# Kernel optimization log

Measured on AMD Instinct MI355X. Metric: run time of the kernel, lower is better.

## Reference

```python
import jax, jax.numpy as jnp
import numpy as np

NB = 4          # bits per symbol (QAM16)
K = 3           # num_streams
M = 8           # rx antennas
B = 4096        # batch
NPTS = 2 ** NB  # constellation points per stream
C = NPTS ** K   # exhaustive candidate vectors


def _pam_gray(b):
    if len(b) > 1:
        return (1 - 2 * b[0]) * (2 ** len(b[1:]) - _pam_gray(b[1:]))
    return 1 - 2 * b[0]


def _qam_points(nb):
    # Gray-labeled QAM, normalized to unit average energy (as sionna's Constellation)
    n = 2 ** nb
    pts = np.zeros(n, np.complex64)
    for i in range(n):
        b = np.array(list(np.binary_repr(i, nb)), int)
        pts[i] = _pam_gray(b[0::2]) + 1j * _pam_gray(b[1::2])
    pts /= np.sqrt(np.mean(np.abs(pts) ** 2)).astype(np.float32)
    return pts.astype(np.complex64)


def _candidates():
    pts = _qam_points(NB)
    idx = np.arange(C)
    # per-stream symbol indices, stream 0 is most significant (vec_list order)
    sym_idx = np.stack([(idx // NPTS ** (K - 1 - k)) % NPTS for k in range(K)], axis=1)  # [C,K]
    xc = pts[sym_idx]  # [C,K] complex candidate symbol vectors
    # bits: MSB-first per symbol -> [C, K, NB]
    bits = ((sym_idx[..., None] >> (NB - 1 - np.arange(NB))) & 1).astype(bool)
    return xc, bits.reshape(C, K * NB)


_XC, _BITS = _candidates()


def setup_inputs() -> dict:
    key = jax.random.key(0)
    ks = jax.random.split(key, 6)
    y_re = jax.random.normal(ks[0], (B, M), jnp.float32)
    y_im = jax.random.normal(ks[1], (B, M), jnp.float32)
    h_re = jax.random.normal(ks[2], (B, M, K), jnp.float32)
    h_im = jax.random.normal(ks[3], (B, M, K), jnp.float32)
    # Hermitian PD noise covariance S = F F^H / M + 2 I
    fr = jax.random.normal(ks[4], (B, M, M), jnp.float32)
    fi = jax.random.normal(ks[5], (B, M, M), jnp.float32)
    F = fr + 1j * fi
    S = jnp.einsum('bij,bkj->bik', F, F.conj()) / M + 2.0 * jnp.eye(M, dtype=jnp.complex64)
    return {"y_re": y_re, "y_im": y_im, "h_re": h_re, "h_im": h_im,
            "s_re": jnp.real(S), "s_im": jnp.imag(S)}


def reference(y_re, y_im, h_re, h_im, s_re, s_im):
    y = y_re + 1j * y_im            # [B,M]
    h = h_re + 1j * h_im            # [B,M,K]
    s = s_re + 1j * s_im            # [B,M,M] Hermitian PD
    # Whiten: L L^H = S ; ||L^{-1}(y - Hx)||^2 = (y-Hx)^H S^{-1} (y-Hx)
    L = jnp.linalg.cholesky(s)
    yw = jax.scipy.linalg.solve_triangular(L, y[..., None], lower=True)[..., 0]  # [B,M]
    hw = jax.scipy.linalg.solve_triangular(L, h, lower=True)                     # [B,M,K]

    xc = jnp.asarray(_XC)                         # [C,K]
    G = jnp.einsum('bmk,bml->bkl', hw.conj(), hw)  # [B,K,K] Gram
    z = jnp.einsum('bm,bmk->bk', yw.conj(), hw)    # [B,K]  y~^H H~
    P = xc.conj()[:, :, None] * xc[:, None, :]     # [C,K,K] candidate outer products
    quad = jnp.real(jnp.einsum('bkl,ckl->bc', G, P))   # x^H G x
    cross = jnp.real(jnp.einsum('bk,ck->bc', z, xc))   # Re(y~^H H~ x)
    yn = jnp.sum(jnp.abs(yw) ** 2, axis=-1, keepdims=True)
    d = yn - 2.0 * cross + quad                   # [B,C] exhaustive squared distances

    # maxlog bit LLRs: LLR = min_{bit=0} d - min_{bit=1} d
    bits = jnp.asarray(_BITS)                     # [C, K*NB] bool
    BIG = jnp.float32(1e30)
    llrs = []
    for p in range(K * NB):  # fixed small loop over bit positions
        mask = bits[:, p]
        min1 = jnp.min(jnp.where(mask, d, BIG), axis=1)
        min0 = jnp.min(jnp.where(mask, BIG, d), axis=1)
        llrs.append(min0 - min1)
    return jnp.stack(llrs, axis=-1).reshape(B, K, NB)
```

## Files before the change

kernel.cpp:

```cpp
#include <hip/hip_runtime.h>
#include <math.h>

#define BIG 1e30f
#define RT10 0.31622776601683794f

__device__ __forceinline__ constexpr float QR(int i) {
    return ((((i >> 3) & 1) ? -1.0f : 1.0f) * ((((i >> 1) & 1) ? 3.0f : 1.0f)) * RT10);
}
__device__ __forceinline__ constexpr float QI(int i) {
    return ((((i >> 2) & 1) ? -1.0f : 1.0f) * (((i & 1) ? 3.0f : 1.0f)) * RT10);
}

__global__ __launch_bounds__(256) void mld_wave(
    const float* __restrict__ y_re, const float* __restrict__ y_im,
    const float* __restrict__ h_re, const float* __restrict__ h_im,
    const float* __restrict__ s_re, const float* __restrict__ s_im,
    float* __restrict__ out, int B) {
    int tid = threadIdx.x;
    int w = tid >> 6, lane = tid & 63;
    int b = blockIdx.x * 4 + w;
    bool live = (b < B);
    if (!live) b = B - 1;

    __shared__ float s_xr[4][4][8], s_xi[4][4][8];
    __shared__ float s_w[4][16];
    __shared__ float s16[4][16];

    {
        int ii = lane >> 3, kk = lane & 7;
        float ar = s_re[b * 64 + lane];
        float ai = s_im[b * 64 + lane];
        float br = 0.0f, bi = 0.0f;
        if (kk == 0) {
            br = y_re[b * 8 + ii];
            bi = y_im[b * 8 + ii];
        } else if (kk < 4) {
            br = h_re[b * 24 + ii * 3 + (kk - 1)];
            bi = h_im[b * 24 + ii * 3 + (kk - 1)];
        }

#pragma unroll
        for (int j = 0; j < 8; ++j) {
            float djr = __shfl(ar, j * 9, 64);
            float dinv = 1.0f / sqrtf(djr);
            if (kk == j && ii >= j) { ar *= dinv; ai *= dinv; }
            float Lijr = __shfl(ar, ii * 8 + j, 64), Liji = __shfl(ai, ii * 8 + j, 64);
            float Lkjr = __shfl(ar, kk * 8 + j, 64), Lkji = __shfl(ai, kk * 8 + j, 64);
            if (kk > j && ii >= kk) {
                ar -= Lijr * Lkjr + Liji * Lkji;
                ai -= Liji * Lkjr - Lijr * Lkji;
            }
        }
#pragma unroll
        for (int k = 0; k < 8; ++k) {
            float dk = __shfl(ar, k * 9, 64);
            float dinvk = 1.0f / dk;
            if (ii == k) { br *= dinvk; bi *= dinvk; }
            float xkr = __shfl(br, k * 8 + kk, 64), xki = __shfl(bi, k * 8 + kk, 64);
            float Likr = __shfl(ar, ii * 8 + k, 64), Liki = __shfl(ai, ii * 8 + k, 64);
            if (ii > k) {
                br -= Likr * xkr - Liki * xki;
                bi -= Likr * xki + Liki * xkr;
            }
        }
        if (kk < 4) { s_xr[w][kk][ii] = br; s_xi[w][kk][ii] = bi; }
    }
    __syncthreads();

    if (lane < 9) {
        int pa = (int)((0x000211321ull >> (lane * 4)) & 15ull);
        int pc = (int)((0x321332321ull >> (lane * 4)) & 15ull);
        float sr = 0.0f, si = 0.0f;
#pragma unroll
        for (int m = 0; m < 8; ++m) {
            float xar = s_xr[w][pa][m], xai = s_xi[w][pa][m];
            float xbr = s_xr[w][pc][m], xbi = s_xi[w][pc][m];
            sr += xar * xbr + xai * xbi;
            si += xar * xbi - xai * xbr;
        }
        if (lane < 3) {
            s_w[w][lane] = sr;
        } else {
            int base2 = 3 + (lane - 3) * 2;
            s_w[w][base2] = sr;
            s_w[w][base2 + 1] = si;
        }
    }
    __syncthreads();

    const float* ww = s_w[w];
    float g00 = ww[0], g11 = ww[1], g22 = ww[2];
    float g01r = ww[3], g01i = ww[4], g02r = ww[5], g02i = ww[6];
    float g12r = ww[7], g12i = ww[8];
    float z0r = ww[9], z0i = ww[10], z1r = ww[11], z1i = ww[12];
    float z2r = ww[13], z2i = ww[14];

    int a = lane >> 4, i1 = lane & 15;
    float p1r = QR(i1), p1i = QI(i1);
    float n1 = p1r * p1r + p1i * p1i;
    float a1c = g11 * n1 - 2.0f * (z1r * p1r - z1i * p1i);
    float w1r = g12r * p1r + g12i * p1i;
    float w1i = g12i * p1r - g12r * p1i;
    float mr0 = (a & 2) ? 3.0f * RT10 : RT10;
    float mi0 = (a & 1) ? 3.0f * RT10 : RT10;
    float n0 = mr0 * mr0 + mi0 * mi0;
    float g00n0 = g00 * n0;

    float ch[12];
#pragma unroll
    for (int j = 0; j < 12; ++j) ch[j] = BIG;
    float u[4];
#pragma unroll
    for (int q = 0; q < 4; ++q) {
        float p0r = (q & 2) ? -mr0 : mr0;
        float p0i = (q & 1) ? -mi0 : mi0;
        float a0c = g00n0 - 2.0f * (z0r * p0r - z0i * p0i);
        float crr = p0r * p1r + p0i * p1i;
        float cri = p0r * p1i - p0i * p1r;
        float base = a0c + a1c + 2.0f * (g01r * crr - g01i * cri);
        float w0r = g02r * p0r + g02i * p0i;
        float w0i = g02i * p0r - g02r * p0i;
        float cr = 2.0f * (w0r + w1r - z2r);
        float ci = -2.0f * (w0i + w1i - z2i);
        float bA = fmaf(g22, 0.2f, base);
        float bB = fmaf(g22, 1.0f, base);
        float bC = fmaf(g22, 1.8f, base);
        float pmin = BIG;
#pragma unroll
        for (int i2 = 0; i2 < 16; ++i2) {
            int cls = ((i2 >> 1) & 1) + (i2 & 1);
            float bX = (cls == 0) ? bA : (cls == 1 ? bB : bC);
            float d = fmaf(QI(i2), ci, fmaf(QR(i2), cr, bX));
            pmin = fminf(pmin, d);
            ch[0 + ((i2 >> 3) & 1)] = fminf(ch[0 + ((i2 >> 3) & 1)], d);
            ch[2 + ((i2 >> 2) & 1)] = fminf(ch[2 + ((i2 >> 2) & 1)], d);
            ch[4 + ((i2 >> 1) & 1)] = fminf(ch[4 + ((i2 >> 1) & 1)], d);
            ch[6 + (i2 & 1)]        = fminf(ch[6 + (i2 & 1)], d);
        }
        u[q] = pmin;
    }
    ch[8] = fminf(u[0], u[1]);
    ch[9] = fminf(u[2], u[3]);
    ch[10] = fminf(u[0], u[2]);
    ch[11] = fminf(u[1], u[3]);

#pragma unroll
    for (int j = 0; j < 12; ++j) {
        float v = ch[j];
#pragma unroll
        for (int mask = 1; mask < 64; mask <<= 1) v = fminf(v, __shfl_xor(v, mask, 64));
        ch[j] = v;
    }

    float t1 = fminf(fminf(u[0], u[1]), fminf(u[2], u[3]));
    float r0 = t1;
#pragma unroll
    for (int mask = 1; mask <= 8; mask <<= 1) r0 = fminf(r0, __shfl_xor(r0, mask, 64));
    float r1 = fminf(t1, __shfl_xor(t1, 16, 64));
    r1 = fminf(r1, __shfl_xor(r1, 32, 64));
    if (lane < 16) s16[w][lane] = r1;

    float zv = fminf(r0, __shfl_xor(r0, 16, 64));
    float llr2 = zv - __shfl_xor(zv, 32, 64);
    float yv = fminf(r0, __shfl_xor(r0, 32, 64));
    float llr3 = yv - __shfl_xor(yv, 16, 64);
    __syncthreads();

    if (live) {
        float* ob = out + b * 12;
        if (lane == 0) {
            ob[0] = ch[8] - ch[9];
            ob[1] = ch[10] - ch[11];
            ob[2] = llr2;
            ob[3] = llr3;
        } else if (lane >= 4 && lane < 8) {
            int k = 3 - (lane - 4);
            float m0 = BIG, m1 = BIG;
#pragma unroll
            for (int j = 0; j < 16; ++j) {
                float v = s16[w][j];
                if ((j >> k) & 1) m1 = fminf(m1, v);
                else m0 = fminf(m0, v);
            }
            ob[lane] = m0 - m1;
        } else if (lane >= 8 && lane < 12) {
            int n = lane - 8;
            ob[lane] = ch[n * 2] - ch[n * 2 + 1];
        }
    }
}

extern "C" void kernel_launch(void* const* d_in, const int* in_sizes, int n_in,
                              void* d_out, int out_size, void* d_ws, size_t ws_size,
                              hipStream_t stream) {
    const float* y_re = (const float*)d_in[0];
    const float* y_im = (const float*)d_in[1];
    const float* h_re = (const float*)d_in[2];
    const float* h_im = (const float*)d_in[3];
    const float* s_re = (const float*)d_in[4];
    const float* s_im = (const float*)d_in[5];
    int B = in_sizes[0] / 8;

    mld_wave<<<dim3((B + 3) / 4), dim3(256), 0, stream>>>(y_re, y_im, h_re, h_im,
                                                          s_re, s_im, (float*)d_out, B);
}
```

Measured before the change: 76.66 us.

## Separate innermost QAM search into independent real/imag minima and use fast rcp/rsq

Replaces the 16-point inner enumeration over the third stream's symbol with a closed form. The distance splits into a real-part term and an imaginary-part term, each minimized over the two PAM amplitudes and signs, so the bit-conditioned minima come from a few fmins and abs operations instead of 16 distance evaluations per candidate. Per-candidate constants are hoisted out of the q loop. It also swaps the IEEE divide and sqrt in the Cholesky and triangular solve for hardware rsq/rcp intrinsics, which may slightly change LLR precision.

```diff
diff --git a/kernel.cpp b/kernel.cpp
--- a/kernel.cpp
+++ b/kernel.cpp
@@ -42,7 +42,7 @@
 #pragma unroll
         for (int j = 0; j < 8; ++j) {
             float djr = __shfl(ar, j * 9, 64);
-            float dinv = 1.0f / sqrtf(djr);
+            float dinv = __builtin_amdgcn_rsqf(djr);
             if (kk == j && ii >= j) { ar *= dinv; ai *= dinv; }
             float Lijr = __shfl(ar, ii * 8 + j, 64), Liji = __shfl(ai, ii * 8 + j, 64);
             float Lkjr = __shfl(ar, kk * 8 + j, 64), Lkji = __shfl(ai, kk * 8 + j, 64);
@@ -54,7 +54,7 @@
 #pragma unroll
         for (int k = 0; k < 8; ++k) {
             float dk = __shfl(ar, k * 9, 64);
-            float dinvk = 1.0f / dk;
+            float dinvk = __builtin_amdgcn_rcpf(dk);
             if (ii == k) { br *= dinvk; bi *= dinvk; }
             float xkr = __shfl(br, k * 8 + kk, 64), xki = __shfl(bi, k * 8 + kk, 64);
             float Likr = __shfl(ar, ii * 8 + k, 64), Liki = __shfl(ai, ii * 8 + k, 64);
@@ -104,7 +104,15 @@
     float mr0 = (a & 2) ? 3.0f * RT10 : RT10;
     float mi0 = (a & 1) ? 3.0f * RT10 : RT10;
     float n0 = mr0 * mr0 + mi0 * mi0;
-    float g00n0 = g00 * n0;
+
+    float C0 = fmaf(g00, n0, a1c);
+    float P = 2.0f * mr0 * (g01r * p1r - g01i * p1i - z0r);
+    float Q = 2.0f * mi0 * (g01r * p1i + g01i * p1r + z0i);
+    float cw = 2.0f * (w1r - z2r);
+    float cv = 2.0f * (z2i - w1i);
+    float gr1 = 2.0f * g02r * mr0, gr2 = 2.0f * g02i * mi0;
+    float gi1 = 2.0f * g02i * mr0, gi2 = 2.0f * g02r * mi0;
+    float gA = 0.1f * g22, gB = 0.9f * g22;
 
     float ch[12];
 #pragma unroll
@@ -112,32 +120,31 @@
     float u[4];
 #pragma unroll
     for (int q = 0; q < 4; ++q) {
-        float p0r = (q & 2) ? -mr0 : mr0;
-        float p0i = (q & 1) ? -mi0 : mi0;
-        float a0c = g00n0 - 2.0f * (z0r * p0r - z0i * p0i);
-        float crr = p0r * p1r + p0i * p1i;
-        float cri = p0r * p1i - p0i * p1r;
-        float base = a0c + a1c + 2.0f * (g01r * crr - g01i * cri);
-        float w0r = g02r * p0r + g02i * p0i;
-        float w0i = g02i * p0r - g02r * p0i;
-        float cr = 2.0f * (w0r + w1r - z2r);
-        float ci = -2.0f * (w0i + w1i - z2i);
-        float bA = fmaf(g22, 0.2f, base);
-        float bB = fmaf(g22, 1.0f, base);
-        float bC = fmaf(g22, 1.8f, base);
-        float pmin = BIG;
-#pragma unroll
-        for (int i2 = 0; i2 < 16; ++i2) {
-            int cls = ((i2 >> 1) & 1) + (i2 & 1);
-            float bX = (cls == 0) ? bA : (cls == 1 ? bB : bC);
-            float d = fmaf(QI(i2), ci, fmaf(QR(i2), cr, bX));
-            pmin = fminf(pmin, d);
-            ch[0 + ((i2 >> 3) & 1)] = fminf(ch[0 + ((i2 >> 3) & 1)], d);
-            ch[2 + ((i2 >> 2) & 1)] = fminf(ch[2 + ((i2 >> 2) & 1)], d);
-            ch[4 + ((i2 >> 1) & 1)] = fminf(ch[4 + ((i2 >> 1) & 1)], d);
-            ch[6 + (i2 & 1)]        = fminf(ch[6 + (i2 & 1)], d);
-        }
-        u[q] = pmin;
+        float base = C0 + ((q & 2) ? -P : P) + ((q & 1) ? -Q : Q);
+        float cr = cw + ((q & 2) ? -gr1 : gr1) + ((q & 1) ? -gr2 : gr2);
+        float ci = cv + ((q & 2) ? gi1 : -gi1) + ((q & 1) ? -gi2 : gi2);
+        float u1 = RT10 * cr, u3 = 3.0f * u1;
+        float v1 = RT10 * ci, v3 = 3.0f * v1;
+        float minRp = fminf(gA + u1, gB + u3);
+        float minRm = fminf(gA - u1, gB - u3);
+        float minR1 = gA - fabsf(u1);
+        float minR3 = gB - fabsf(u3);
+        float minR = fminf(minR1, minR3);
+        float minIp = fminf(gA + v1, gB + v3);
+        float minIm = fminf(gA - v1, gB - v3);
+        float minI1 = gA - fabsf(v1);
+        float minI3 = gB - fabsf(v3);
+        float minI = fminf(minI1, minI3);
+        float sR = base + minR, sI = base + minI;
+        ch[0] = fminf(ch[0], sI + minRp);
+        ch[1] = fminf(ch[1], sI + minRm);
+        ch[2] = fminf(ch[2], sR + minIp);
+        ch[3] = fminf(ch[3], sR + minIm);
+        ch[4] = fminf(ch[4], sI + minR1);
+        ch[5] = fminf(ch[5], sI + minR3);
+        ch[6] = fminf(ch[6], sR + minI1);
+        ch[7] = fminf(ch[7], sR + minI3);
+        u[q] = sR + minI;
     }
     ch[8] = fminf(u[0], u[1]);
     ch[9] = fminf(u[2], u[3]);
```

Result: no change. 75.69 us (-1.3%).
